# Kernel tuning notes

Hardware: AMD Instinct MI355X
Metric: run time of the kernel (lower is better)

## Reference

```python
import jax, jax.numpy as jnp
import numpy as np

N_NODES = 50000
N_EDGES = 600000
H = 128


def setup_inputs() -> dict:
    key = jax.random.key(0)
    ks = jax.random.split(key, 7)
    node_emb = jax.random.normal(ks[0], (N_NODES, H), dtype=jnp.float32)
    # PyTorch Linear default init ~ U(-1/sqrt(fan_in), 1/sqrt(fan_in)); scaled normal is fine for a baseline
    W1 = jax.random.normal(ks[1], (H, 2 * H), dtype=jnp.float32) * (1.0 / np.sqrt(2 * H))
    b1 = jax.random.normal(ks[2], (H,), dtype=jnp.float32) * 0.01
    W2 = jax.random.normal(ks[3], (1, H), dtype=jnp.float32) * (1.0 / np.sqrt(H))
    b2 = jax.random.normal(ks[4], (1,), dtype=jnp.float32) * 0.01
    src = jax.random.randint(ks[5], (N_EDGES,), 0, N_NODES, dtype=jnp.int64)
    dst = jax.random.randint(ks[6], (N_EDGES,), 0, N_NODES, dtype=jnp.int64)
    return {"node_emb": node_emb, "W1": W1, "b1": b1, "W2": W2, "b2": b2,
            "src": src, "dst": dst}


def reference(node_emb, W1, b1, W2, b2, src, dst):
    # gather per-edge endpoint embeddings and concat -> [E, 2H]
    h = jnp.concatenate([node_emb[src], node_emb[dst]], axis=1)
    # 2-layer MLP: Linear(2H->H) -> ReLU -> Linear(H->1) -> squeeze
    hidden = jax.nn.relu(h @ W1.T + b1)          # [E, H]
    scores = hidden @ W2.T + b2                   # [E, 1]
    return scores[:, 0]                           # [E]
```

## Files before the change

### kernel.cpp

```cpp
#include <hip/hip_runtime.h>
#include <hip/hip_bf16.h>


#define H   128
#define NJJ 256
#define BM  32
#define EPW 32
#define CPAD_F32 260

typedef __attribute__((ext_vector_type(8))) short  frag_ab;
typedef __attribute__((ext_vector_type(4))) float  f32x4;
typedef __attribute__((ext_vector_type(4))) unsigned int   uint4v;

__device__ __forceinline__ unsigned short f2bf(float x) {
    unsigned int u = __float_as_uint(x);
    unsigned int r = u + 0x7FFFu + ((u >> 16) & 1u);
    return (unsigned short)(r >> 16);
}

__device__ __forceinline__ unsigned int pk_bf16(float lo, float hi) {
    unsigned int r;
    asm("v_cvt_pk_bf16_f32 %0, %1, %2" : "=v"(r) : "v"(lo), "v"(hi));
    return r;
}

__device__ __forceinline__ frag_ab relu_sum(uint4v s, uint4v d) {
    uint4v r;
#pragma unroll
    for (int p = 0; p < 4; ++p) {
        float sl = __uint_as_float(s[p] << 16);
        float sh = __uint_as_float(s[p] & 0xFFFF0000u);
        float dl = __uint_as_float(d[p] << 16);
        float dh = __uint_as_float(d[p] & 0xFFFF0000u);
        float l = sl + dl; l = l > 0.f ? l : 0.f;
        float h = sh + dh; h = h > 0.f ? h : 0.f;
        r[p] = pk_bf16(l, h);
    }
    return __builtin_bit_cast(frag_ab, r);
}

__global__ __launch_bounds__(256)
void convert_weights(const float* __restrict__ W1, const float* __restrict__ W2,
                     unsigned short* __restrict__ W1f, unsigned short* __restrict__ W2c) {
    if (blockIdx.x == 128) {
        if (threadIdx.x < H) W2c[threadIdx.x] = f2bf(W2[threadIdx.x]);
        return;
    }
    int idx = blockIdx.x * 256 + threadIdx.x;
    int e     = idx & 7;
    int chunk = idx >> 3;
    int lane  = chunk & 63;
    int ks    = (chunk >> 6) & 3;
    int cf    = (chunk >> 8) & 3;
    int wid   = chunk >> 10;
    int col   = wid * 64 + (lane & 15) + cf * 16;
    int k     = ks * 32 + (lane >> 4) * 8 + e;
    W1f[idx] = f2bf(W1[(size_t)(col & 127) * 256 + (size_t)(col >> 7) * H + k]);
}

__device__ __forceinline__ int swz_chunk(int c, int row) {
    return (c & ~7) | ((c ^ row) & 7);
}

__global__ __launch_bounds__(256)
void precompute_P_mfma(const float* __restrict__ emb,
                       const unsigned short* __restrict__ W1f,
                       const float* __restrict__ b1,
                       unsigned short* __restrict__ P,
                       int n_nodes) {
    __shared__ __align__(1024) float ldsbuf[BM * CPAD_F32];
    float* ldsA = ldsbuf;
    float* ldsC = ldsbuf;

    int tid  = threadIdx.x;
    int lane = tid & 63;
    int wid  = tid >> 6;
    int block0 = blockIdx.x * BM;
    if (block0 + BM > n_nodes) block0 = n_nodes - BM;
    if (block0 < 0) block0 = 0;

    const frag_ab* wf = (const frag_ab*)W1f;
    frag_ab Bf[4][4];
#pragma unroll
    for (int cf = 0; cf < 4; ++cf)
#pragma unroll
        for (int ks = 0; ks < 4; ++ks)
            Bf[cf][ks] = wf[(((size_t)wid * 4 + cf) * 4 + ks) * 64 + lane];

    {
#pragma unroll
        for (int j = 0; j < 4; ++j) {
            int row = wid * 8 + j * 2 + (lane >> 5);
            int cp  = lane & 31;
            int c   = swz_chunk(cp, row);
            const float* g = emb + (size_t)(block0 + row) * H + c * 4;
            void* l = (char*)ldsA + wid * 4096 + j * 1024;
            __builtin_amdgcn_global_load_lds(
                (const __attribute__((address_space(1))) void*)g,
                (__attribute__((address_space(3))) void*)l, 16, 0, 0);
        }
    }
    __syncthreads();

    f32x4 acc[2][4];
#pragma unroll
    for (int mf = 0; mf < 2; ++mf)
#pragma unroll
        for (int cf = 0; cf < 4; ++cf) acc[mf][cf] = (f32x4){0.f, 0.f, 0.f, 0.f};

    int row16 = lane & 15;
    int g4    = lane >> 4;
#pragma unroll
    for (int ks = 0; ks < 4; ++ks) {
        frag_ab Af[2];
#pragma unroll
        for (int mf = 0; mf < 2; ++mf) {
            int row   = mf * 16 + row16;
            int cbase = ks * 8 + g4 * 2;
            const char* base = (const char*)ldsA + row * 512;
            float4 x = *(const float4*)(base + (swz_chunk(cbase,     row) << 4));
            float4 y = *(const float4*)(base + (swz_chunk(cbase + 1, row) << 4));
            uint4v w;
            w[0] = pk_bf16(x.x, x.y);
            w[1] = pk_bf16(x.z, x.w);
            w[2] = pk_bf16(y.x, y.y);
            w[3] = pk_bf16(y.z, y.w);
            Af[mf] = __builtin_bit_cast(frag_ab, w);
        }
#pragma unroll
        for (int mf = 0; mf < 2; ++mf)
#pragma unroll
            for (int cf = 0; cf < 4; ++cf)
                acc[mf][cf] = __builtin_amdgcn_mfma_f32_16x16x32_bf16(
                    Af[mf], Bf[cf][ks], acc[mf][cf], 0, 0, 0);
    }

    __syncthreads();

    {
        int colbase = wid * 64 + row16;
        int rbase   = g4 * 4;
        float b1c[4];
#pragma unroll
        for (int cf = 0; cf < 4; ++cf) {
            int col = colbase + cf * 16;
            b1c[cf] = (col < H) ? b1[col] : 0.f;
        }
#pragma unroll
        for (int mf = 0; mf < 2; ++mf)
#pragma unroll
            for (int cf = 0; cf < 4; ++cf) {
                int col = colbase + cf * 16;
#pragma unroll
                for (int r = 0; r < 4; ++r) {
                    int row = mf * 16 + rbase + r;
                    ldsC[row * CPAD_F32 + col] = acc[mf][cf][r] + b1c[cf];
                }
            }
    }
    __syncthreads();

#pragma unroll
    for (int it = 0; it < 4; ++it) {
        int c   = it * 256 + tid;
        int row = c >> 5;
        int off = c & 31;
        const float4* s = (const float4*)(ldsC + row * CPAD_F32 + off * 8);
        float4 x = s[0], y = s[1];
        uint4v o;
        o[0] = pk_bf16(x.x, x.y);
        o[1] = pk_bf16(x.z, x.w);
        o[2] = pk_bf16(y.x, y.y);
        o[3] = pk_bf16(y.z, y.w);
        *(uint4v*)((char*)P + (size_t)(block0 + row) * 512 + off * 16) = o;
    }
}

__global__ __launch_bounds__(256)
void edge_score_mfma(const unsigned short* __restrict__ P,
                     const unsigned short* __restrict__ W2c,
                     const float* __restrict__ b2,
                     const int* __restrict__ src,
                     const int* __restrict__ dst,
                     float* __restrict__ out,
                     int n_edges) {
    int lane = threadIdx.x & 63;
    int wave = blockIdx.x * 4 + (threadIdx.x >> 6);
    int e0 = wave * EPW;
    if (e0 >= n_edges) return;

    frag_ab Bf[4];
    {
        int krun = (lane >> 4) * 8;
#pragma unroll
        for (int ks = 0; ks < 4; ++ks)
            Bf[ks] = *(const frag_ab*)(W2c + ks * 32 + krun);
    }
    float b2v = b2[0];
    int el = lane & 15;
    int kb = (lane >> 4) * 16;

    int eA = e0 + el;       if (eA > n_edges - 1) eA = n_edges - 1;
    int eB = e0 + 16 + el;  if (eB > n_edges - 1) eB = n_edges - 1;
    const char* pb = (const char*)P;
    const char* sA = pb + (size_t)src[eA] * 512 + kb;
    const char* dA = pb + (size_t)dst[eA] * 512 + 256 + kb;
    const char* sB = pb + (size_t)src[eB] * 512 + kb;
    const char* dB = pb + (size_t)dst[eB] * 512 + 256 + kb;

    uint4v rsA[4], rdA[4], rsB[4], rdB[4];
#pragma unroll
    for (int ks = 0; ks < 4; ++ks) {
        rsA[ks] = *(const uint4v*)(sA + ks * 64);
        rdA[ks] = *(const uint4v*)(dA + ks * 64);
        rsB[ks] = *(const uint4v*)(sB + ks * 64);
        rdB[ks] = *(const uint4v*)(dB + ks * 64);
    }

    f32x4 accA = (f32x4){0.f, 0.f, 0.f, 0.f};
    f32x4 accB = (f32x4){0.f, 0.f, 0.f, 0.f};
#pragma unroll
    for (int ks = 0; ks < 4; ++ks) {
        accA = __builtin_amdgcn_mfma_f32_16x16x32_bf16(relu_sum(rsA[ks], rdA[ks]), Bf[ks], accA, 0, 0, 0);
        accB = __builtin_amdgcn_mfma_f32_16x16x32_bf16(relu_sum(rsB[ks], rdB[ks]), Bf[ks], accB, 0, 0, 0);
    }

    if (el == 0) {
        int r0 = (lane >> 4) * 4;
        int ea = e0 + r0, eb = e0 + 16 + r0;
        float4 oA = { accA[0] + b2v, accA[1] + b2v, accA[2] + b2v, accA[3] + b2v };
        float4 oB = { accB[0] + b2v, accB[1] + b2v, accB[2] + b2v, accB[3] + b2v };
        if (eb + 3 < n_edges) {
            *(float4*)(out + ea) = oA;
            *(float4*)(out + eb) = oB;
        } else {
#pragma unroll
            for (int r = 0; r < 4; ++r) {
                if (ea + r < n_edges) out[ea + r] = accA[r] + b2v;
                if (eb + r < n_edges) out[eb + r] = accB[r] + b2v;
            }
        }
    }
}

__global__ __launch_bounds__(128)
void naive_edge(const float* __restrict__ emb,
                const float* __restrict__ W1,
                const float* __restrict__ b1,
                const float* __restrict__ W2,
                const float* __restrict__ b2,
                const int* __restrict__ src,
                const int* __restrict__ dst,
                float* __restrict__ out,
                int n_edges) {
    __shared__ float es[H], ed[H];
    __shared__ float red[2];
    int e = blockIdx.x;
    if (e >= n_edges) return;
    int j = threadIdx.x;
    int s = src[e], d = dst[e];
    es[j] = emb[(size_t)s * H + j];
    ed[j] = emb[(size_t)d * H + j];
    __syncthreads();
    const float* w = W1 + (size_t)j * 256;
    float acc = b1[j];
    for (int k = 0; k < H; ++k) acc += es[k] * w[k] + ed[k] * w[H + k];
    acc = acc > 0.f ? acc : 0.f;
    float p = acc * W2[j];
#pragma unroll
    for (int off = 32; off; off >>= 1) p += __shfl_xor(p, off, 64);
    int lane = j & 63, wid = j >> 6;
    if (lane == 0) red[wid] = p;
    __syncthreads();
    if (j == 0) out[e] = red[0] + red[1] + b2[0];
}

extern "C" void kernel_launch(void* const* d_in, const int* in_sizes, int n_in,
                              void* d_out, int out_size, void* d_ws, size_t ws_size,
                              hipStream_t stream) {
    const float* emb = (const float*)d_in[0];
    const float* W1  = (const float*)d_in[1];
    const float* b1  = (const float*)d_in[2];
    const float* W2  = (const float*)d_in[3];
    const float* b2  = (const float*)d_in[4];
    const int*   src = (const int*)d_in[5];
    const int*   dst = (const int*)d_in[6];
    float* out = (float*)d_out;

    int n_nodes = in_sizes[0] / H;
    int n_edges = in_sizes[5];

    size_t needP = (size_t)n_nodes * NJJ * sizeof(unsigned short);
    size_t offW1 = (needP + 255) & ~(size_t)255;
    size_t offW2 = offW1 + (size_t)NJJ * H * sizeof(unsigned short);
    size_t need  = offW2 + 256;

    if (ws_size >= need && n_nodes >= BM) {
        unsigned short* P   = (unsigned short*)d_ws;
        unsigned short* W1f = (unsigned short*)((char*)d_ws + offW1);
        unsigned short* W2c = (unsigned short*)((char*)d_ws + offW2);
        convert_weights<<<129, 256, 0, stream>>>(W1, W2, W1f, W2c);
        int grid1 = (n_nodes + BM - 1) / BM;
        precompute_P_mfma<<<grid1, 256, 0, stream>>>(emb, W1f, b1, P, n_nodes);
        int grid2 = (n_edges + EPW * 4 - 1) / (EPW * 4);
        edge_score_mfma<<<grid2, 256, 0, stream>>>(P, W2c, b2, src, dst, out, n_edges);
    } else {
        naive_edge<<<n_edges, 128, 0, stream>>>(emb, W1, b1, W2, b2, src, dst, out, n_edges);
    }
}
```

Baseline: 64.41 us.

## Store P directly from MFMA registers in permuted layout, prefetch W1 fragments

The precompute kernel drops the LDS staging pass for its output. Each lane now writes its accumulator values straight to global P as packed 8-byte stores, in a permuted column order within each 64-column group. W2c is permuted to match, so the edge kernel's dot product stays consistent. W1 fragments are also double-buffered across the k-loop (which is no longer unrolled) instead of all being loaded up front. The goal is to cut LDS traffic, two barriers and register pressure, at the cost of narrower, less coalesced global stores and a possible load stall inside the loop.

```diff
diff --git a/kernel.cpp b/kernel.cpp
--- a/kernel.cpp
+++ b/kernel.cpp
@@ -6,11 +6,11 @@
 #define NJJ 256
 #define BM  32
 #define EPW 32
-#define CPAD_F32 260
 
 typedef __attribute__((ext_vector_type(8))) short  frag_ab;
 typedef __attribute__((ext_vector_type(4))) float  f32x4;
 typedef __attribute__((ext_vector_type(4))) unsigned int   uint4v;
+typedef __attribute__((ext_vector_type(2))) unsigned int   uint2v;
 
 __device__ __forceinline__ unsigned short f2bf(float x) {
     unsigned int u = __float_as_uint(x);
@@ -43,7 +43,11 @@
 void convert_weights(const float* __restrict__ W1, const float* __restrict__ W2,
                      unsigned short* __restrict__ W1f, unsigned short* __restrict__ W2c) {
     if (blockIdx.x == 128) {
-        if (threadIdx.x < H) W2c[threadIdx.x] = f2bf(W2[threadIdx.x]);
+        int j = threadIdx.x;
+        if (j < H) {
+            int pos = (j >> 6) * 64 + 4 * (j & 15) + ((j & 63) >> 4);
+            W2c[pos] = f2bf(W2[j]);
+        }
         return;
     }
     int idx = blockIdx.x * 256 + threadIdx.x;
@@ -68,24 +72,13 @@
                        const float* __restrict__ b1,
                        unsigned short* __restrict__ P,
                        int n_nodes) {
-    __shared__ __align__(1024) float ldsbuf[BM * CPAD_F32];
-    float* ldsA = ldsbuf;
-    float* ldsC = ldsbuf;
-
+    __shared__ __align__(1024) float ldsA[BM * H];
     int tid  = threadIdx.x;
     int lane = tid & 63;
     int wid  = tid >> 6;
     int block0 = blockIdx.x * BM;
     if (block0 + BM > n_nodes) block0 = n_nodes - BM;
     if (block0 < 0) block0 = 0;
-
-    const frag_ab* wf = (const frag_ab*)W1f;
-    frag_ab Bf[4][4];
-#pragma unroll
-    for (int cf = 0; cf < 4; ++cf)
-#pragma unroll
-        for (int ks = 0; ks < 4; ++ks)
-            Bf[cf][ks] = wf[(((size_t)wid * 4 + cf) * 4 + ks) * 64 + lane];
 
     {
 #pragma unroll
@@ -100,18 +93,38 @@
                 (__attribute__((address_space(3))) void*)l, 16, 0, 0);
         }
     }
-    __syncthreads();
-
-    f32x4 acc[2][4];
-#pragma unroll
-    for (int mf = 0; mf < 2; ++mf)
-#pragma unroll
-        for (int cf = 0; cf < 4; ++cf) acc[mf][cf] = (f32x4){0.f, 0.f, 0.f, 0.f};
 
     int row16 = lane & 15;
     int g4    = lane >> 4;
-#pragma unroll
+
+    float b1c[4];
+#pragma unroll
+    for (int cf = 0; cf < 4; ++cf) {
+        int col = wid * 64 + cf * 16 + row16;
+        b1c[cf] = (col < H) ? b1[col] : 0.f;
+    }
+
+    const frag_ab* wf = (const frag_ab*)W1f;
+    f32x4 acc[2][4];
+#pragma unroll
+    for (int mf = 0; mf < 2; ++mf)
+#pragma unroll
+        for (int cf = 0; cf < 4; ++cf) acc[mf][cf] = (f32x4){0.f, 0.f, 0.f, 0.f};
+
+    frag_ab Bcur[4], Bnxt[4];
+#pragma unroll
+    for (int cf = 0; cf < 4; ++cf)
+        Bcur[cf] = wf[((wid * 4 + cf) * 4 + 0) * 64 + lane];
+
+    __syncthreads();
+
+#pragma unroll 1
     for (int ks = 0; ks < 4; ++ks) {
+        if (ks < 3) {
+#pragma unroll
+            for (int cf = 0; cf < 4; ++cf)
+                Bnxt[cf] = wf[((wid * 4 + cf) * 4 + ks + 1) * 64 + lane];
+        }
         frag_ab Af[2];
 #pragma unroll
         for (int mf = 0; mf < 2; ++mf) {
@@ -132,48 +145,23 @@
 #pragma unroll
             for (int cf = 0; cf < 4; ++cf)
                 acc[mf][cf] = __builtin_amdgcn_mfma_f32_16x16x32_bf16(
-                    Af[mf], Bf[cf][ks], acc[mf][cf], 0, 0, 0);
-    }
-
-    __syncthreads();
-
-    {
-        int colbase = wid * 64 + row16;
-        int rbase   = g4 * 4;
-        float b1c[4];
-#pragma unroll
-        for (int cf = 0; cf < 4; ++cf) {
-            int col = colbase + cf * 16;
-            b1c[cf] = (col < H) ? b1[col] : 0.f;
-        }
-#pragma unroll
-        for (int mf = 0; mf < 2; ++mf)
-#pragma unroll
-            for (int cf = 0; cf < 4; ++cf) {
-                int col = colbase + cf * 16;
-#pragma unroll
-                for (int r = 0; r < 4; ++r) {
-                    int row = mf * 16 + rbase + r;
-                    ldsC[row * CPAD_F32 + col] = acc[mf][cf][r] + b1c[cf];
-                }
-            }
-    }
-    __syncthreads();
-
-#pragma unroll
-    for (int it = 0; it < 4; ++it) {
-        int c   = it * 256 + tid;
-        int row = c >> 5;
-        int off = c & 31;
-        const float4* s = (const float4*)(ldsC + row * CPAD_F32 + off * 8);
-        float4 x = s[0], y = s[1];
-        uint4v o;
-        o[0] = pk_bf16(x.x, x.y);
-        o[1] = pk_bf16(x.z, x.w);
-        o[2] = pk_bf16(y.x, y.y);
-        o[3] = pk_bf16(y.z, y.w);
-        *(uint4v*)((char*)P + (size_t)(block0 + row) * 512 + off * 16) = o;
-    }
+                    Af[mf], Bcur[cf], acc[mf][cf], 0, 0, 0);
+        if (ks < 3) {
+#pragma unroll
+            for (int cf = 0; cf < 4; ++cf) Bcur[cf] = Bnxt[cf];
+        }
+    }
+
+#pragma unroll
+    for (int mf = 0; mf < 2; ++mf)
+#pragma unroll
+        for (int r = 0; r < 4; ++r) {
+            int row = block0 + mf * 16 + g4 * 4 + r;
+            uint2v v;
+            v[0] = pk_bf16(acc[mf][0][r] + b1c[0], acc[mf][1][r] + b1c[1]);
+            v[1] = pk_bf16(acc[mf][2][r] + b1c[2], acc[mf][3][r] + b1c[3]);
+            *(uint2v*)((char*)P + (size_t)row * 512 + wid * 128 + 8 * row16) = v;
+        }
 }
 
 __global__ __launch_bounds__(256)
```

Result: no change. 64.50 us, median of 2 (+0.1%).
